# Performance work log

Hardware: AMD Instinct MI355X
Metric: run time of the kernel (lower is better)

## Reference

```python
import jax, jax.numpy as jnp
import numpy as np

NHEAD = 16
D_MODEL = 1024
D_K = D_MODEL // NHEAD


def setup_inputs() -> dict:
    key = jax.random.key(0)
    ks = jax.random.split(key, 12)
    B, S, D = 2, 2048, D_MODEL
    scale = 1.0 / np.sqrt(D)
    inp = {
        "value": jax.random.normal(ks[0], (B, S, D), dtype=jnp.float32),
        "key": jax.random.normal(ks[1], (B, S, D), dtype=jnp.float32),
        "query": jax.random.normal(ks[2], (B, S, D), dtype=jnp.float32),
        "mask": jax.random.randint(ks[3], (B, 1, S, S), 0, 2, dtype=jnp.int32),
        "Wv": jax.random.normal(ks[4], (D, D), dtype=jnp.float32) * scale,
        "bv": jnp.zeros((D,), dtype=jnp.float32),
        "Wk": jax.random.normal(ks[5], (D, D), dtype=jnp.float32) * scale,
        "bk": jnp.zeros((D,), dtype=jnp.float32),
        "Wq": jax.random.normal(ks[6], (D, D), dtype=jnp.float32) * scale,
        "bq": jnp.zeros((D,), dtype=jnp.float32),
        "Wo": jax.random.normal(ks[7], (D, D), dtype=jnp.float32) * scale,
        "bo": jnp.zeros((D,), dtype=jnp.float32),
    }
    return inp


def reference(value, key, query, mask, Wv, bv, Wk, bk, Wq, bq, Wo, bo):
    B, S, D = value.shape
    H, Dk = NHEAD, D_K

    def proj(x, W, b):
        # nn.Linear: x @ W^T + b, then split heads -> [B, H, S, Dk]
        return (x @ W.T + b).reshape(B, S, H, Dk).transpose(0, 2, 1, 3)

    v = proj(value, Wv, bv)
    k = proj(key, Wk, bk)
    q = proj(query, Wq, bq)

    # NOTE: source code swaps K and V when calling attention():
    #   scores = Q @ V^T / sqrt(d_k);  out = softmax(scores) @ K
    scores = jnp.einsum("bhqd,bhkd->bhqk", q, v) / jnp.sqrt(jnp.float32(Dk))
    scores = jnp.where(mask == 0, jnp.float32(-1e9), scores)
    attn = jax.nn.softmax(scores, axis=-1)  # [B, H, S, S]
    attr_value = jnp.einsum("bhqk,bhkd->bhqd", attn, k)

    out = attr_value.transpose(0, 2, 1, 3).reshape(B, S, H * Dk)
    return out @ Wo.T + bo
```

## Files before the change

### kernel.cpp

```cpp
#include <hip/hip_runtime.h>

#define S_LEN 2048
#define DMODEL 1024
#define NHEADS 16
#define DKH 64

typedef __attribute__((ext_vector_type(8))) short bf16x8;
typedef __attribute__((ext_vector_type(4))) short bf16x4;
typedef __attribute__((ext_vector_type(4))) float f32x4;

#if __has_builtin(__builtin_amdgcn_exp2f)
#define EXP2F(x) __builtin_amdgcn_exp2f(x)
#define QSCALE (0.125f * 1.44269504f)
#else
#define EXP2F(x) __expf(x)
#define QSCALE 0.125f
#endif

static __device__ __forceinline__ short f2bf(float f) {
    unsigned b = __float_as_uint(f);
    b = (b + 0x7FFFu + ((b >> 16) & 1u)) >> 16;
    return (short)b;
}

static __device__ __forceinline__ unsigned pktrunc(float lo, float hi) {
#if __has_builtin(__builtin_amdgcn_perm)
    return __builtin_amdgcn_perm(__float_as_uint(hi), __float_as_uint(lo), 0x07060302u);
#else
    return (__float_as_uint(lo) >> 16) | (__float_as_uint(hi) & 0xFFFF0000u);
#endif
}

static __device__ __forceinline__ f32x4 mfma16(bf16x8 a, bf16x8 b, f32x4 c) {
    return __builtin_amdgcn_mfma_f32_16x16x32_bf16(a, b, c, 0, 0, 0);
}

static __device__ __forceinline__ f32x4 mfma_k16(bf16x4 a, bf16x4 b, f32x4 c) {
    return __builtin_amdgcn_mfma_f32_16x16x16bf16_1k(a, b, c, 0, 0, 0);
}

static __device__ __forceinline__ void glds16(const short* g, short* l) {
    __builtin_amdgcn_global_load_lds(
        (const __attribute__((address_space(1))) void*)g,
        (__attribute__((address_space(3))) void*)l, 16, 0, 0);
}

struct CvtArgs { const float* src[7]; short* dst[7]; };

__global__ __launch_bounds__(256) void prep(CvtArgs a, const int* __restrict__ mask,
                                            unsigned long long* __restrict__ mw) {
    if (blockIdx.x < 8192) {
        const size_t i8 = ((size_t)blockIdx.x * 256 + threadIdx.x) * 8;
        int seg; size_t off;
        if (i8 < ((size_t)12 << 20)) { seg = (int)(i8 >> 22); off = i8 & ((1u << 22) - 1); }
        else { size_t r = i8 - ((size_t)12 << 20); seg = 3 + (int)(r >> 20); off = r & ((1u << 20) - 1); }
        const float* s = a.src[seg] + off;
        float4 x0 = *(const float4*)s, x1 = *(const float4*)(s + 4);
        short o[8];
        o[0] = f2bf(x0.x); o[1] = f2bf(x0.y); o[2] = f2bf(x0.z); o[3] = f2bf(x0.w);
        o[4] = f2bf(x1.x); o[5] = f2bf(x1.y); o[6] = f2bf(x1.z); o[7] = f2bf(x1.w);
        *(uint4*)(a.dst[seg] + off) = *(uint4*)o;
    } else {
        const int wv = ((blockIdx.x - 8192) << 2) + (threadIdx.x >> 6);
        const int lane = threadIdx.x & 63;
        const size_t base = (size_t)wv << 4;
        #pragma unroll 4
        for (int it = 0; it < 16; ++it) {
            const size_t w = base + it;
            const int m = mask[(w << 6) + lane];
            unsigned long long bal = __ballot(m != 0);
            if (lane == 0) mw[w] = bal;
        }
    }
}

struct GemmArgs { const short* X[3]; const short* W[3]; const float* B[3];
                  void* C[3]; float scale[3]; };

template <int MODE>
__global__ __launch_bounds__(256) void gemm_bt(GemmArgs a) {
    __shared__ short Ah[128 * 32];
    __shared__ short Bh[128 * 32];
    const int z = blockIdx.z;
    const short* X = a.X[z];
    const short* W = a.W[z];
    const float* bias = a.B[z];
    const float scl = a.scale[z];

    const int t = threadIdx.x, wid = t >> 6, lane = t & 63;
    const int l15 = lane & 15, lq = lane >> 4;
    int m0, n0;
    if (MODE == 0 && z == 2) { m0 = blockIdx.y << 7; n0 = blockIdx.x << 7; }
    else                     { m0 = blockIdx.x << 7; n0 = blockIdx.y << 7; }
    const int wm = (wid >> 1) << 6, wn = (wid & 1) << 6;

    const int kb = (lane & 3) ^ ((lane >> 3) & 3);
    const int r0 = (wid << 5) + (lane >> 2);
    const short* ag0 = X + (size_t)(m0 + r0) * 1024 + (kb << 3);
    const short* ag1 = ag0 + 16 * 1024;
    const short* bg0 = W + (size_t)(n0 + r0) * 1024 + (kb << 3);
    const short* bg1 = bg0 + 16 * 1024;
    short* lA0 = Ah + (wid << 5) * 32;
    short* lA1 = lA0 + 16 * 32;
    short* lB0 = Bh + (wid << 5) * 32;
    short* lB1 = lB0 + 16 * 32;

    const int fpos = (lq ^ ((l15 >> 1) & 3)) << 3;

    f32x4 acc[4][4] = {};

    for (int k0 = 0; k0 < 1024; k0 += 32) {
        __syncthreads();
        glds16(ag0, lA0); glds16(ag1, lA1);
        glds16(bg0, lB0); glds16(bg1, lB1);
        ag0 += 32; ag1 += 32; bg0 += 32; bg1 += 32;
        __syncthreads();

        bf16x8 af[4], bfr[4];
        #pragma unroll
        for (int i = 0; i < 4; ++i)
            af[i] = *(const bf16x8*)&Ah[(wm + i * 16 + l15) * 32 + fpos];
        #pragma unroll
        for (int j = 0; j < 4; ++j)
            bfr[j] = *(const bf16x8*)&Bh[(wn + j * 16 + l15) * 32 + fpos];
        #pragma unroll
        for (int i = 0; i < 4; ++i)
            #pragma unroll
            for (int j = 0; j < 4; ++j)
                acc[i][j] = mfma16(af[i], bfr[j], acc[i][j]);
    }

    if (MODE == 0 && z == 2) {
        #pragma unroll
        for (int i = 0; i < 4; ++i) {
            #pragma unroll
            for (int r = 0; r < 4; ++r) {
                const int o = m0 + wm + i * 16 + (lq << 2) + r;
                const float bo_ = bias[o];
                const int h = o >> 6, d = o & 63;
                #pragma unroll
                for (int j = 0; j < 4; ++j) {
                    const int n = n0 + wn + j * 16 + l15;
                    const int bb = n >> 11, s = n & 2047;
                    ((short*)a.C[2])[(((size_t)((bb * 16 + h) << 6) + d) << 11) + s] =
                        f2bf(acc[i][j][r] + bo_);
                }
            }
        }
        return;
    }

    #pragma unroll
    for (int j = 0; j < 4; ++j) {
        const int n = n0 + wn + j * 16 + l15;
        const float bn = bias[n];
        #pragma unroll
        for (int i = 0; i < 4; ++i) {
            const int mbase = m0 + wm + i * 16 + (lq << 2);
            #pragma unroll
            for (int r = 0; r < 4; ++r) {
                const float val = (acc[i][j][r] + bn) * scl;
                const int m = mbase + r;
                if (MODE == 0) {
                    const int b = m >> 11, s = m & 2047, h = n >> 6, d = n & 63;
                    ((short*)a.C[z])[((((size_t)(b * 16 + h)) << 11) + s) * 64 + d] = f2bf(val);
                } else {
                    ((float*)a.C[z])[((size_t)m << 10) + n] = val;
                }
            }
        }
    }
}

__global__ __launch_bounds__(256, 4) void attn4(
    const short* __restrict__ Qh, const short* __restrict__ Vh,
    const short* __restrict__ Kt, const unsigned long long* __restrict__ MW,
    short* __restrict__ Opart, float* __restrict__ lpart)
{
    __shared__ short Vs[64 * 64];
    __shared__ short Ks[64 * 64];

    const int t = threadIdx.x, wid = t >> 6, lane = t & 63;
    const int l15 = lane & 15, lq = lane >> 4;
    const int bh = blockIdx.y, b = bh >> 4;
    const int z = blockIdx.z;
    const int ib = (blockIdx.x << 7) + (wid << 5);
    const int jbase = z << 10;

    bf16x8 qf[2][2];
    #pragma unroll
    for (int it = 0; it < 2; ++it) {
        const short* qp = Qh + ((size_t)bh * 2048 + ib + it * 16 + l15) * 64 + (lq << 3);
        qf[it][0] = *(const bf16x8*)qp;
        qf[it][1] = *(const bf16x8*)(qp + 32);
    }

    const int sr = lane >> 3, pc = lane & 7;
    const int lc = pc ^ sr;
    const int wr = wid << 4;
    const short* vsrc = Vh + (size_t)bh * 131072 + (size_t)(jbase + wr + sr) * 64 + (lc << 3);
    const short* ksrc = Kt + (size_t)bh * 131072 + (size_t)(wr + sr) * 2048 + jbase + (lc << 3);
    short* vdst = Vs + (wr << 6);
    short* kdst = Ks + (wr << 6);

    const unsigned long long* mwp0 = MW + ((size_t)b * 2048 + ib + l15) * 32 + (z << 4);
    const unsigned long long* mwp1 = mwp0 + (size_t)16 * 32;

    const int x7 = l15 & 7;
    int voff[2], koff[4];
    #pragma unroll
    for (int p = 0; p < 2; ++p) voff[p] = (((p << 2) + lq) ^ x7) << 3;
    #pragma unroll
    for (int jt = 0; jt < 4; ++jt) {
        const int c8 = (jt << 2) + lq;
        koff[jt] = (((c8 >> 1) ^ x7) << 3) + ((c8 & 1) << 2);
    }

    f32x4 O[2][4] = {};
    f32x4 lsum[2] = {};
    bf16x4 ones;
    #pragma unroll
    for (int e = 0; e < 4; ++e) ones[e] = (short)0x3F80;

    for (int jc = 0; jc < 16; ++jc) {
        __syncthreads();
        glds16(vsrc, vdst);
        glds16(vsrc + 512, vdst + 512);
        glds16(ksrc, kdst);
        glds16(ksrc + 8 * 2048, kdst + 512);
        vsrc += 4096; ksrc += 64;

        uint2 mword[2];
        mword[0] = *(const uint2*)(mwp0 + jc);
        mword[1] = *(const uint2*)(mwp1 + jc);
        __syncthreads();

        bf16x8 vf[4][2];
        #pragma unroll
        for (int jt = 0; jt < 4; ++jt) {
            const short* vp = &Vs[((jt << 4) + l15) << 6];
            vf[jt][0] = *(const bf16x8*)(vp + voff[0]);
            vf[jt][1] = *(const bf16x8*)(vp + voff[1]);
        }

        bf16x4 paf[2][4];
        #pragma unroll
        for (int it = 0; it < 2; ++it) {
            const unsigned wx = mword[it].x, wy = mword[it].y;
            #pragma unroll
            for (int jt = 0; jt < 4; ++jt) {
                f32x4 sc = {};
                sc = mfma16(vf[jt][0], qf[it][0], sc);
                sc = mfma16(vf[jt][1], qf[it][1], sc);
                const unsigned w32 = (jt < 2) ? wx : wy;
                float p[4];
                #pragma unroll
                for (int r = 0; r < 4; ++r) {
                    const unsigned bit = (w32 >> (((jt & 1) << 4) + (lq << 2) + r)) & 1u;
                    const float e = EXP2F(sc[r]);
                    p[r] = bit ? e : 0.f;
                }
                uint2 uu;
                uu.x = pktrunc(p[0], p[1]);
                uu.y = pktrunc(p[2], p[3]);
                paf[it][jt] = __builtin_bit_cast(bf16x4, uu);
                lsum[it] = mfma_k16(paf[it][jt], ones, lsum[it]);
            }
        }

        #pragma unroll
        for (int dt = 0; dt < 4; ++dt) {
            const short* kp = &Ks[((dt << 4) + l15) << 6];
            #pragma unroll
            for (int jt = 0; jt < 4; ++jt) {
                const bf16x4 kfv = *(const bf16x4*)(kp + koff[jt]);
                O[0][dt] = mfma_k16(paf[0][jt], kfv, O[0][dt]);
                O[1][dt] = mfma_k16(paf[1][jt], kfv, O[1][dt]);
            }
        }
    }

    const size_t zb = (size_t)((z << 5) + bh) * 2048;
    #pragma unroll
    for (int it = 0; it < 2; ++it) {
        const int rb = ib + (it << 4) + (lq << 2);
        if (l15 == 0) {
            #pragma unroll
            for (int r = 0; r < 4; ++r)
                lpart[zb + rb + r] = lsum[it][r];
        }
        #pragma unroll
        for (int dt = 0; dt < 4; ++dt)
            #pragma unroll
            for (int r = 0; r < 4; ++r)
                Opart[(zb + rb + r) * 64 + (dt << 4) + l15] = f2bf(O[it][dt][r]);
    }
}

__global__ __launch_bounds__(256) void combine(const short* __restrict__ Op,
                                               const float* __restrict__ lp,
                                               short* __restrict__ attr) {
    const int idx = blockIdx.x * 256 + threadIdx.x;
    const int d8 = (idx & 7) << 3;
    const int srow = (idx >> 3) & 2047;
    const int bh = idx >> 14, b = bh >> 4, h = bh & 15;
    const size_t r0 = (size_t)bh * 2048 + srow;
    const size_t r1 = r0 + (size_t)32 * 2048;
    uint4 a = *(const uint4*)(Op + r0 * 64 + d8);
    uint4 c = *(const uint4*)(Op + r1 * 64 + d8);
    const float inv = 1.f / (lp[r0] + lp[r1]);
    const unsigned* au = (const unsigned*)&a;
    const unsigned* cu = (const unsigned*)&c;
    short o[8];
    #pragma unroll
    for (int i = 0; i < 4; ++i) {
        const float a0 = __uint_as_float(au[i] << 16);
        const float a1 = __uint_as_float(au[i] & 0xFFFF0000u);
        const float c0 = __uint_as_float(cu[i] << 16);
        const float c1 = __uint_as_float(cu[i] & 0xFFFF0000u);
        o[2 * i + 0] = f2bf((a0 + c0) * inv);
        o[2 * i + 1] = f2bf((a1 + c1) * inv);
    }
    *(uint4*)&attr[((size_t)b * 2048 + srow) * 1024 + (h << 6) + d8] = *(uint4*)o;
}

extern "C" void kernel_launch(void* const* d_in, const int* in_sizes, int n_in,
                              void* d_out, int out_size, void* d_ws, size_t ws_size,
                              hipStream_t stream) {
    const float* value = (const float*)d_in[0];
    const float* key   = (const float*)d_in[1];
    const float* query = (const float*)d_in[2];
    const int*   mask  = (const int*)d_in[3];
    const float* bv = (const float*)d_in[5];
    const float* bk = (const float*)d_in[7];
    const float* bq = (const float*)d_in[9];
    const float* bo = (const float*)d_in[11];
    float* out = (float*)d_out;

    const size_t M1 = (size_t)1 << 20, M4 = (size_t)1 << 22;
    short* ws = (short*)d_ws;
    short* Xq = ws;
    short* Xk = ws + M4;
    short* Xv = ws + 2 * M4;
    short* Wc0 = ws + 3 * M4;
    short* Wc1 = Wc0 + M1;
    short* Wc2 = Wc1 + M1;
    short* Wc3 = Wc2 + M1;
    short* qh = ws + 4 * M4;
    short* kt = ws + 5 * M4;
    short* vh = ws + 6 * M4;
    unsigned long long* maskw = (unsigned long long*)(ws + 7 * M4);
    short* attr = Xq;
    short* Opart = Xk;
    float* lpart = (float*)Wc0;

    CvtArgs cv;
    cv.src[0] = query; cv.dst[0] = Xq;
    cv.src[1] = key;   cv.dst[1] = Xk;
    cv.src[2] = value; cv.dst[2] = Xv;
    cv.src[3] = (const float*)d_in[8];  cv.dst[3] = Wc0;
    cv.src[4] = (const float*)d_in[6];  cv.dst[4] = Wc1;
    cv.src[5] = (const float*)d_in[4];  cv.dst[5] = Wc2;
    cv.src[6] = (const float*)d_in[10]; cv.dst[6] = Wc3;
    prep<<<10240, 256, 0, stream>>>(cv, mask, maskw);

    GemmArgs g1;
    g1.X[0] = Xq;  g1.W[0] = Wc0; g1.B[0] = bq; g1.C[0] = qh; g1.scale[0] = QSCALE;
    g1.X[1] = Xv;  g1.W[1] = Wc2; g1.B[1] = bv; g1.C[1] = vh; g1.scale[1] = 1.f;
    g1.X[2] = Wc1; g1.W[2] = Xk;  g1.B[2] = bk; g1.C[2] = kt; g1.scale[2] = 1.f;
    gemm_bt<0><<<dim3(32, 8, 3), 256, 0, stream>>>(g1);

    attn4<<<dim3(16, 32, 2), 256, 0, stream>>>(qh, vh, kt, maskw, Opart, lpart);

    combine<<<2048, 256, 0, stream>>>(Opart, lpart, attr);

    GemmArgs g2;
    g2.X[0] = attr; g2.W[0] = Wc3; g2.B[0] = bo; g2.C[0] = out; g2.scale[0] = 1.f;
    g2.X[1] = attr; g2.W[1] = Wc3; g2.B[1] = bo; g2.C[1] = out; g2.scale[1] = 1.f;
    g2.X[2] = attr; g2.W[2] = Wc3; g2.B[2] = bo; g2.C[2] = out; g2.scale[2] = 1.f;
    gemm_bt<1><<<dim3(32, 8, 1), 256, 0, stream>>>(g2);
}
```

Measured before the change: 271.2 us.

## Double-buffer V/K LDS tiles and prefetch mask words in attention loop

Converts the attention kernel's single LDS buffers for V and K into two buffers. The next chunk's global-to-LDS loads and mask words are issued before computing on the current chunk, with explicit vmcnt waits and raw barriers in place of __syncthreads. It also replaces the per-element mask bit test and select with a shift-based bitmask AND on the exp result. The aim is to overlap global load latency with MFMA work, at the cost of double the LDS footprint, which may reduce occupancy under launch_bounds(256,4). It also relies on hand-counted vmcnt values being correct.

```diff
diff --git a/kernel.cpp b/kernel.cpp
--- a/kernel.cpp
+++ b/kernel.cpp
@@ -177,8 +177,8 @@
     const short* __restrict__ Kt, const unsigned long long* __restrict__ MW,
     short* __restrict__ Opart, float* __restrict__ lpart)
 {
-    __shared__ short Vs[64 * 64];
-    __shared__ short Ks[64 * 64];
+    __shared__ short Vs[2][64 * 64];
+    __shared__ short Ks[2][64 * 64];
 
     const int t = threadIdx.x, wid = t >> 6, lane = t & 63;
     const int l15 = lane & 15, lq = lane >> 4;
@@ -200,8 +200,8 @@
     const int wr = wid << 4;
     const short* vsrc = Vh + (size_t)bh * 131072 + (size_t)(jbase + wr + sr) * 64 + (lc << 3);
     const short* ksrc = Kt + (size_t)bh * 131072 + (size_t)(wr + sr) * 2048 + jbase + (lc << 3);
-    short* vdst = Vs + (wr << 6);
-    short* kdst = Ks + (wr << 6);
+    short* vdst0 = &Vs[0][wr << 6];
+    short* kdst0 = &Ks[0][wr << 6];
 
     const unsigned long long* mwp0 = MW + ((size_t)b * 2048 + ib + l15) * 32 + (z << 4);
     const unsigned long long* mwp1 = mwp0 + (size_t)16 * 32;
@@ -222,23 +222,42 @@
     #pragma unroll
     for (int e = 0; e < 4; ++e) ones[e] = (short)0x3F80;
 
+    const int lsh = lq << 2;
+
+#define STAGE(nb) do {                                          \
+        short* vd_ = vdst0 + ((nb) << 12);                      \
+        short* kd_ = kdst0 + ((nb) << 12);                      \
+        glds16(vsrc, vd_); glds16(vsrc + 512, vd_ + 512);       \
+        glds16(ksrc, kd_); glds16(ksrc + 8 * 2048, kd_ + 512);  \
+        vsrc += 4096; ksrc += 64;                               \
+    } while (0)
+
+    uint2 mc0 = *(const uint2*)mwp0;
+    uint2 mc1 = *(const uint2*)mwp1;
+    STAGE(0);
+
+    #pragma unroll 2
     for (int jc = 0; jc < 16; ++jc) {
-        __syncthreads();
-        glds16(vsrc, vdst);
-        glds16(vsrc + 512, vdst + 512);
-        glds16(ksrc, kdst);
-        glds16(ksrc + 8 * 2048, kdst + 512);
-        vsrc += 4096; ksrc += 64;
-
-        uint2 mword[2];
-        mword[0] = *(const uint2*)(mwp0 + jc);
-        mword[1] = *(const uint2*)(mwp1 + jc);
-        __syncthreads();
+        const int cur = jc & 1;
+        uint2 mn0 = {}, mn1 = {};
+        if (jc < 15) {
+            mn0 = *(const uint2*)(mwp0 + jc + 1);
+            mn1 = *(const uint2*)(mwp1 + jc + 1);
+            STAGE(cur ^ 1);
+            asm volatile("s_waitcnt vmcnt(6)" ::: "memory");
+        } else {
+            asm volatile("s_waitcnt vmcnt(0)" ::: "memory");
+        }
+        __builtin_amdgcn_s_barrier();
+        asm volatile("" ::: "memory");
+
+        const short* Vb = &Vs[cur][0];
+        const short* Kb = &Ks[cur][0];
 
         bf16x8 vf[4][2];
         #pragma unroll
         for (int jt = 0; jt < 4; ++jt) {
-            const short* vp = &Vs[((jt << 4) + l15) << 6];
+            const short* vp = Vb + (((jt << 4) + l15) << 6);
             vf[jt][0] = *(const bf16x8*)(vp + voff[0]);
             vf[jt][1] = *(const bf16x8*)(vp + voff[1]);
         }
@@ -246,19 +265,22 @@
         bf16x4 paf[2][4];
         #pragma unroll
         for (int it = 0; it < 2; ++it) {
-            const unsigned wx = mword[it].x, wy = mword[it].y;
+            const uint2 mwv = it ? mc1 : mc0;
+            const unsigned wxs = mwv.x >> lsh;
+            const unsigned wys = mwv.y >> lsh;
             #pragma unroll
             for (int jt = 0; jt < 4; ++jt) {
                 f32x4 sc = {};
                 sc = mfma16(vf[jt][0], qf[it][0], sc);
                 sc = mfma16(vf[jt][1], qf[it][1], sc);
-                const unsigned w32 = (jt < 2) ? wx : wy;
+                const unsigned ws = (jt < 2) ? wxs : wys;
                 float p[4];
                 #pragma unroll
                 for (int r = 0; r < 4; ++r) {
-                    const unsigned bit = (w32 >> (((jt & 1) << 4) + (lq << 2) + r)) & 1u;
+                    const int pos = ((jt & 1) << 4) + r;
+                    const unsigned bm = (unsigned)(((int)(ws << (31 - pos))) >> 31);
                     const float e = EXP2F(sc[r]);
-                    p[r] = bit ? e : 0.f;
+                    p[r] = __uint_as_float(__float_as_uint(e) & bm);
                 }
                 uint2 uu;
                 uu.x = pktrunc(p[0], p[1]);
@@ -270,7 +292,7 @@
 
         #pragma unroll
         for (int dt = 0; dt < 4; ++dt) {
-            const short* kp = &Ks[((dt << 4) + l15) << 6];
+            const short* kp = Kb + (((dt << 4) + l15) << 6);
             #pragma unroll
             for (int jt = 0; jt < 4; ++jt) {
                 const bf16x4 kfv = *(const bf16x4*)(kp + koff[jt]);
@@ -278,7 +300,12 @@
                 O[1][dt] = mfma_k16(paf[1][jt], kfv, O[1][dt]);
             }
         }
-    }
+
+        asm volatile("" ::: "memory");
+        __builtin_amdgcn_s_barrier();
+        mc0 = mn0; mc1 = mn1;
+    }
+#undef STAGE
 
     const size_t zb = (size_t)((z << 5) + bh) * 2048;
     #pragma unroll
```

Result: no change. 272.7 us (+0.6%).
